# Kernel optimization log

Measured on AMD Instinct MI355X. Metric: run time of the kernel, lower is better.

Reference implementation:

```python
import jax, jax.numpy as jnp
import numpy as np

N = 100_000      # nodes
DEG = 16         # avg in-degree (fixed per node for setup)
E = N * DEG      # edges
IN = 256         # in_feats
H = 4            # num_heads
D = 64           # out_feats per head
NEG_SLOPE = 0.2


def setup_inputs() -> dict:
    key = jax.random.key(0)
    k1, k2, k3, k4, k5 = jax.random.split(key, 5)
    # dst-major CSR with uniform degree DEG per destination node
    row_ptr = jnp.arange(N + 1, dtype=jnp.int32) * DEG          # [N+1]
    col_ind = jax.random.randint(k1, (E,), 0, N, dtype=jnp.int32)  # source ids per edge
    feat = jax.random.normal(k2, (N, IN), dtype=jnp.float32)
    # fc.weight (xavier-ish scale), torch Linear: y = x @ W.T
    W = jax.random.normal(k3, (H * D, IN), dtype=jnp.float32) * (1.0 / np.sqrt(IN))
    attn_l = jax.random.normal(k4, (1, H, D), dtype=jnp.float32) * 0.1
    attn_r = jax.random.normal(k5, (1, H, D), dtype=jnp.float32) * 0.1
    return {"row_ptr": row_ptr, "col_ind": col_ind, "feat": feat,
            "W": W, "attn_l": attn_l, "attn_r": attn_r}


def reference(row_ptr, col_ind, feat, W, attn_l, attn_r):
    n_nodes = feat.shape[0]
    n_edges = col_ind.shape[0]
    # feat_src = feat_dst = fc(feat).view(-1, H, D)
    feat_src = (feat @ W.T).reshape(n_nodes, H, D)
    el = jnp.sum(feat_src * attn_l, axis=-1)   # [N, H]
    er = jnp.sum(feat_src * attn_r, axis=-1)   # [N, H]
    # per-edge dst id from CSR row_ptr; src = col_ind
    dst = (jnp.searchsorted(row_ptr, jnp.arange(n_edges, dtype=row_ptr.dtype),
                            side='right') - 1).astype(jnp.int32)
    src = col_ind
    # e = u_add_v(g, er, el) -> er[src] + el[dst], then LeakyReLU
    e = er[src] + el[dst]                      # [E, H]
    e = jnp.where(e > 0, e, NEG_SLOPE * e)
    # CSR edge-softmax: normalize over incoming edges of each dst row
    m = jax.ops.segment_max(e, dst, num_segments=n_nodes)    # [N, H]
    ex = jnp.exp(e - m[dst])
    s = jax.ops.segment_sum(ex, dst, num_segments=n_nodes)   # [N, H]
    a = ex / s[dst]                                          # [E, H]
    # multi-head SpMM: out[n,h] = sum_{e: dst=n} a[e,h] * feat_src[src[e],h]
    outs = []
    for h in range(H):  # small fixed head loop to avoid [E,H,D] intermediate
        msg = a[:, h, None] * feat_src[src, h]               # [E, D]
        outs.append(jax.ops.segment_sum(msg, dst, num_segments=n_nodes))
    return jnp.stack(outs, axis=1)                           # [N, H, D]
```

## Files before the change

### kernel.cpp

```cpp
#include <hip/hip_runtime.h>
#include <math.h>


#define HEADS 4
#define KIN 256
#define NOUT 256
#define NEG_SLOPE 0.2f
#define BK 32
#define SA 40
#define SB 40

typedef __attribute__((ext_vector_type(4))) short short4v;
typedef __attribute__((ext_vector_type(8))) short short8v;
typedef __attribute__((ext_vector_type(4))) float floatx4;

static __device__ __forceinline__ unsigned short f2bf(float x) {
  unsigned u = __float_as_uint(x);
  u += 0x7FFFu + ((u >> 16) & 1u);
  return (unsigned short)(u >> 16);
}
static __device__ __forceinline__ float bf2f(unsigned short b) {
  return __uint_as_float(((unsigned)b) << 16);
}

__global__ __launch_bounds__(256) void k_cast_w(const float* __restrict__ W,
                                                unsigned short* __restrict__ Wbf) {
  const int i = blockIdx.x * 256 + threadIdx.x;
  float4 f = ((const float4*)W)[i];
  ushort4 o;
  o.x = f2bf(f.x); o.y = f2bf(f.y); o.z = f2bf(f.z); o.w = f2bf(f.w);
  ((ushort4*)Wbf)[i] = o;
}

__global__ __launch_bounds__(256) void k_gemm_mfma(
    const float* __restrict__ feat, const unsigned short* __restrict__ Wbf,
    const float* __restrict__ attn_l, const float* __restrict__ attn_r,
    unsigned short* __restrict__ fs_bf, float* __restrict__ el,
    float* __restrict__ er, int n_nodes) {
  __shared__ unsigned short Alds[64 * SA];
  __shared__ unsigned short Blds[256 * SB];

  const int tid = threadIdx.x;
  const int lane = tid & 63;
  const int w = tid >> 6;
  const int m0 = blockIdx.x * 64;
  const int q = lane >> 4;
  const int l15 = lane & 15;

  floatx4 acc[4][4];
#pragma unroll
  for (int mt = 0; mt < 4; ++mt)
#pragma unroll
    for (int nt = 0; nt < 4; ++nt)
#pragma unroll
      for (int r = 0; r < 4; ++r) acc[mt][nt][r] = 0.0f;

  const int a_row = tid >> 3;
  const int a_kk = (tid & 7) * 4;

  for (int kc = 0; kc < 8; ++kc) {
    const int k0 = kc * BK;
#pragma unroll
    for (int half = 0; half < 2; ++half) {
      const int row = a_row + half * 32;
      int gr = m0 + row;
      if (gr >= n_nodes) gr = n_nodes - 1;
      float4 f = *(const float4*)(feat + (size_t)gr * KIN + k0 + a_kk);
      uint2 p;
      p.x = ((unsigned)f2bf(f.y) << 16) | f2bf(f.x);
      p.y = ((unsigned)f2bf(f.w) << 16) | f2bf(f.z);
      *(uint2*)(&Alds[row * SA + a_kk]) = p;
    }
    {
      const uint4* src = (const uint4*)(Wbf + (size_t)tid * KIN + k0);
      uint2* dst = (uint2*)(&Blds[tid * SB]);
#pragma unroll
      for (int i = 0; i < 4; ++i) {
        uint4 v = src[i];
        dst[2 * i + 0] = make_uint2(v.x, v.y);
        dst[2 * i + 1] = make_uint2(v.z, v.w);
      }
    }
    __syncthreads();
    short8v af[4], bfr[4];
#pragma unroll
    for (int mt = 0; mt < 4; ++mt) {
      const unsigned short* p = &Alds[(mt * 16 + l15) * SA + q * 8];
      short4v lo = *(const short4v*)p;
      short4v hi = *(const short4v*)(p + 4);
      af[mt] = __builtin_shufflevector(lo, hi, 0, 1, 2, 3, 4, 5, 6, 7);
    }
#pragma unroll
    for (int nt = 0; nt < 4; ++nt) {
      const unsigned short* p = &Blds[(w * 64 + nt * 16 + l15) * SB + q * 8];
      short4v lo = *(const short4v*)p;
      short4v hi = *(const short4v*)(p + 4);
      bfr[nt] = __builtin_shufflevector(lo, hi, 0, 1, 2, 3, 4, 5, 6, 7);
    }
#pragma unroll
    for (int mt = 0; mt < 4; ++mt)
#pragma unroll
      for (int nt = 0; nt < 4; ++nt)
        acc[mt][nt] = __builtin_amdgcn_mfma_f32_16x16x32_bf16(
            af[mt], bfr[nt], acc[mt][nt], 0, 0, 0);
    __syncthreads();
  }

  float alv[4], arv[4];
#pragma unroll
  for (int nt = 0; nt < 4; ++nt) {
    alv[nt] = attn_l[w * 64 + nt * 16 + l15];
    arv[nt] = attn_r[w * 64 + nt * 16 + l15];
  }
#pragma unroll
  for (int mt = 0; mt < 4; ++mt) {
#pragma unroll
    for (int r = 0; r < 4; ++r) {
      const int m = m0 + mt * 16 + q * 4 + r;
      const bool mvalid = (m < n_nodes);
      float pl = 0.f, pr = 0.f;
#pragma unroll
      for (int nt = 0; nt < 4; ++nt) {
        const float v = acc[mt][nt][r];
        pl = fmaf(v, alv[nt], pl);
        pr = fmaf(v, arv[nt], pr);
        if (mvalid)
          fs_bf[(size_t)m * NOUT + w * 64 + nt * 16 + l15] = f2bf(v);
      }
#pragma unroll
      for (int off = 1; off < 16; off <<= 1) {
        pl += __shfl_xor(pl, off, 64);
        pr += __shfl_xor(pr, off, 64);
      }
      if (l15 == 0 && mvalid) {
        el[m * HEADS + w] = pl;
        er[m * HEADS + w] = pr;
      }
    }
  }
}

__global__ __launch_bounds__(256) void k_aggregate(
    const int* __restrict__ row_ptr, const int* __restrict__ col_ind,
    const float* __restrict__ el, const float* __restrict__ er,
    const unsigned short* __restrict__ fs_bf, float* __restrict__ out,
    int n_nodes) {
  const int gid = blockIdx.x * blockDim.x + threadIdx.x;
  const int node = gid >> 6;
  const int lane = threadIdx.x & 63;
  if (node >= n_nodes) return;

  const int h = lane >> 4;
  const int j = lane & 15;
  const int rs = row_ptr[node];
  const int deg = row_ptr[node + 1] - rs;

  const bool valid = (j < deg);
  const int src = valid ? col_ind[rs + j] : 0;

  float e = valid ? (er[src * HEADS + h] + el[node * HEADS + h]) : -INFINITY;
  e = (e > 0.f) ? e : NEG_SLOPE * e;

  float mx = e;
#pragma unroll
  for (int off = 1; off < 16; off <<= 1) mx = fmaxf(mx, __shfl_xor(mx, off, 64));
  float ex = valid ? __expf(e - mx) : 0.f;
  float s = ex;
#pragma unroll
  for (int off = 1; off < 16; off <<= 1) s += __shfl_xor(s, off, 64);
  const float a = ex / s;

  const ushort4* __restrict__ fs4 = (const ushort4*)fs_bf;
  const int hbase = lane & 48;
  float4 acc = make_float4(0.f, 0.f, 0.f, 0.f);
#pragma unroll
  for (int j2 = 0; j2 < 16; ++j2) {
    const int sj = __shfl(src, j2, 64);
    const float wgt = __shfl(a, hbase + j2, 64);
    const ushort4 u = fs4[(size_t)sj * (NOUT / 4) + lane];
    acc.x = fmaf(wgt, bf2f(u.x), acc.x);
    acc.y = fmaf(wgt, bf2f(u.y), acc.y);
    acc.z = fmaf(wgt, bf2f(u.z), acc.z);
    acc.w = fmaf(wgt, bf2f(u.w), acc.w);
  }
  ((float4*)out)[(size_t)node * (NOUT / 4) + lane] = acc;
}

extern "C" void kernel_launch(void* const* d_in, const int* in_sizes, int n_in,
                              void* d_out, int out_size, void* d_ws, size_t ws_size,
                              hipStream_t stream) {
  const int* row_ptr = (const int*)d_in[0];
  const int* col_ind = (const int*)d_in[1];
  const float* feat = (const float*)d_in[2];
  const float* W = (const float*)d_in[3];
  const float* attn_l = (const float*)d_in[4];
  const float* attn_r = (const float*)d_in[5];
  float* out = (float*)d_out;
  const int n_nodes = in_sizes[0] - 1;

  char* ws = (char*)d_ws;
  unsigned short* Wbf = (unsigned short*)ws;
  unsigned short* fs_bf = (unsigned short*)(ws + 128 * 1024);
  size_t fs_bytes = (size_t)n_nodes * NOUT * sizeof(unsigned short);
  float* el = (float*)(ws + 128 * 1024 + fs_bytes);
  float* er = el + (size_t)n_nodes * HEADS;

  k_cast_w<<<64, 256, 0, stream>>>(W, Wbf);
  k_gemm_mfma<<<(n_nodes + 63) / 64, 256, 0, stream>>>(
      feat, Wbf, attn_l, attn_r, fs_bf, el, er, n_nodes);
  k_aggregate<<<(n_nodes + 3) / 4, 256, 0, stream>>>(
      row_ptr, col_ind, el, er, fs_bf, out, n_nodes);
}
```

Measured before the change: 360.4 us.

## Restructure GEMM to per-wave 16-row tiles with direct global operand loads

The projection GEMM no longer stages A and B through LDS with block barriers. Each wave now owns 16 rows and computes all 256 output columns, loading feat rows and bf16 W fragments straight from global memory (W should stay cache-resident). Results are staged through a per-wave LDS buffer so fs_bf is written with coalesced 16-byte stores, and el/er are computed for all heads per wave. The aggregate kernel's output store becomes nontemporal, and launch bounds request two blocks per CU. The risk is higher register pressure from 16 accumulators and repeated W loads from L2 for every wave.

```diff
diff --git a/kernel.cpp b/kernel.cpp
--- a/kernel.cpp
+++ b/kernel.cpp
@@ -6,11 +6,8 @@
 #define KIN 256
 #define NOUT 256
 #define NEG_SLOPE 0.2f
-#define BK 32
-#define SA 40
-#define SB 40
+#define SR 280
 
-typedef __attribute__((ext_vector_type(4))) short short4v;
 typedef __attribute__((ext_vector_type(8))) short short8v;
 typedef __attribute__((ext_vector_type(4))) float floatx4;
 
@@ -32,111 +29,95 @@
   ((ushort4*)Wbf)[i] = o;
 }
 
-__global__ __launch_bounds__(256) void k_gemm_mfma(
+__global__ __launch_bounds__(256, 2) void k_gemm_mfma(
     const float* __restrict__ feat, const unsigned short* __restrict__ Wbf,
     const float* __restrict__ attn_l, const float* __restrict__ attn_r,
     unsigned short* __restrict__ fs_bf, float* __restrict__ el,
     float* __restrict__ er, int n_nodes) {
-  __shared__ unsigned short Alds[64 * SA];
-  __shared__ unsigned short Blds[256 * SB];
+  __shared__ unsigned short R[4 * 16 * SR];
 
   const int tid = threadIdx.x;
   const int lane = tid & 63;
   const int w = tid >> 6;
-  const int m0 = blockIdx.x * 64;
   const int q = lane >> 4;
   const int l15 = lane & 15;
+  const int m0 = blockIdx.x * 64 + w * 16;
 
-  floatx4 acc[4][4];
+  int arow_i = m0 + l15;
+  if (arow_i >= n_nodes) arow_i = n_nodes - 1;
+  const float* __restrict__ arow = feat + (size_t)arow_i * KIN;
+
+  floatx4 acc[16];
 #pragma unroll
-  for (int mt = 0; mt < 4; ++mt)
+  for (int nt = 0; nt < 16; ++nt) acc[nt] = (floatx4)0.f;
+
 #pragma unroll
-    for (int nt = 0; nt < 4; ++nt)
+  for (int kc = 0; kc < 8; ++kc) {
+    const int k0 = kc * 32 + q * 8;
+    float4 a0 = *(const float4*)(arow + k0);
+    float4 a1 = *(const float4*)(arow + k0 + 4);
+    short8v af;
+    af[0] = f2bf(a0.x); af[1] = f2bf(a0.y); af[2] = f2bf(a0.z); af[3] = f2bf(a0.w);
+    af[4] = f2bf(a1.x); af[5] = f2bf(a1.y); af[6] = f2bf(a1.z); af[7] = f2bf(a1.w);
 #pragma unroll
-      for (int r = 0; r < 4; ++r) acc[mt][nt][r] = 0.0f;
-
-  const int a_row = tid >> 3;
-  const int a_kk = (tid & 7) * 4;
-
-  for (int kc = 0; kc < 8; ++kc) {
-    const int k0 = kc * BK;
-#pragma unroll
-    for (int half = 0; half < 2; ++half) {
-      const int row = a_row + half * 32;
-      int gr = m0 + row;
-      if (gr >= n_nodes) gr = n_nodes - 1;
-      float4 f = *(const float4*)(feat + (size_t)gr * KIN + k0 + a_kk);
-      uint2 p;
-      p.x = ((unsigned)f2bf(f.y) << 16) | f2bf(f.x);
-      p.y = ((unsigned)f2bf(f.w) << 16) | f2bf(f.z);
-      *(uint2*)(&Alds[row * SA + a_kk]) = p;
+    for (int nt = 0; nt < 16; ++nt) {
+      short8v bf = *(const short8v*)(Wbf + (size_t)(nt * 16 + l15) * KIN + k0);
+      acc[nt] = __builtin_amdgcn_mfma_f32_16x16x32_bf16(af, bf, acc[nt], 0, 0, 0);
     }
-    {
-      const uint4* src = (const uint4*)(Wbf + (size_t)tid * KIN + k0);
-      uint2* dst = (uint2*)(&Blds[tid * SB]);
-#pragma unroll
-      for (int i = 0; i < 4; ++i) {
-        uint4 v = src[i];
-        dst[2 * i + 0] = make_uint2(v.x, v.y);
-        dst[2 * i + 1] = make_uint2(v.z, v.w);
-      }
-    }
-    __syncthreads();
-    short8v af[4], bfr[4];
-#pragma unroll
-    for (int mt = 0; mt < 4; ++mt) {
-      const unsigned short* p = &Alds[(mt * 16 + l15) * SA + q * 8];
-      short4v lo = *(const short4v*)p;
-      short4v hi = *(const short4v*)(p + 4);
-      af[mt] = __builtin_shufflevector(lo, hi, 0, 1, 2, 3, 4, 5, 6, 7);
-    }
-#pragma unroll
-    for (int nt = 0; nt < 4; ++nt) {
-      const unsigned short* p = &Blds[(w * 64 + nt * 16 + l15) * SB + q * 8];
-      short4v lo = *(const short4v*)p;
-      short4v hi = *(const short4v*)(p + 4);
-      bfr[nt] = __builtin_shufflevector(lo, hi, 0, 1, 2, 3, 4, 5, 6, 7);
-    }
-#pragma unroll
-    for (int mt = 0; mt < 4; ++mt)
-#pragma unroll
-      for (int nt = 0; nt < 4; ++nt)
-        acc[mt][nt] = __builtin_amdgcn_mfma_f32_16x16x32_bf16(
-            af[mt], bfr[nt], acc[mt][nt], 0, 0, 0);
-    __syncthreads();
   }
 
-  float alv[4], arv[4];
+  float al_[16], ar_[16];
 #pragma unroll
-  for (int nt = 0; nt < 4; ++nt) {
-    alv[nt] = attn_l[w * 64 + nt * 16 + l15];
-    arv[nt] = attn_r[w * 64 + nt * 16 + l15];
+  for (int nt = 0; nt < 16; ++nt) {
+    al_[nt] = attn_l[nt * 16 + l15];
+    ar_[nt] = attn_r[nt * 16 + l15];
   }
 #pragma unroll
-  for (int mt = 0; mt < 4; ++mt) {
+  for (int r = 0; r < 4; ++r) {
+    const int m = m0 + q * 4 + r;
+    float pl[HEADS], pr[HEADS];
 #pragma unroll
-    for (int r = 0; r < 4; ++r) {
-      const int m = m0 + mt * 16 + q * 4 + r;
-      const bool mvalid = (m < n_nodes);
-      float pl = 0.f, pr = 0.f;
+    for (int h = 0; h < HEADS; ++h) {
+      pl[h] = 0.f; pr[h] = 0.f;
 #pragma unroll
-      for (int nt = 0; nt < 4; ++nt) {
-        const float v = acc[mt][nt][r];
-        pl = fmaf(v, alv[nt], pl);
-        pr = fmaf(v, arv[nt], pr);
-        if (mvalid)
-          fs_bf[(size_t)m * NOUT + w * 64 + nt * 16 + l15] = f2bf(v);
+      for (int t = 0; t < 4; ++t) {
+        const int nt = h * 4 + t;
+        const float v = acc[nt][r];
+        pl[h] = fmaf(v, al_[nt], pl[h]);
+        pr[h] = fmaf(v, ar_[nt], pr[h]);
       }
 #pragma unroll
       for (int off = 1; off < 16; off <<= 1) {
-        pl += __shfl_xor(pl, off, 64);
-        pr += __shfl_xor(pr, off, 64);
-      }
-      if (l15 == 0 && mvalid) {
-        el[m * HEADS + w] = pl;
-        er[m * HEADS + w] = pr;
+        pl[h] += __shfl_xor(pl[h], off, 64);
+        pr[h] += __shfl_xor(pr[h], off, 64);
       }
     }
+    if (m < n_nodes && l15 < HEADS) {
+      float vl = pl[0], vr = pr[0];
+      if (l15 == 1) { vl = pl[1]; vr = pr[1]; }
+      else if (l15 == 2) { vl = pl[2]; vr = pr[2]; }
+      else if (l15 == 3) { vl = pl[3]; vr = pr[3]; }
+      el[m * HEADS + l15] = vl;
+      er[m * HEADS + l15] = vr;
+    }
+  }
+
+  unsigned short* Rw = &R[w * 16 * SR];
+#pragma unroll
+  for (int nt = 0; nt < 16; ++nt)
+#pragma unroll
+    for (int r = 0; r < 4; ++r)
+      Rw[(q * 4 + r) * SR + nt * 16 + l15] = f2bf(acc[nt][r]);
+
+  const int rrow = lane >> 5;
+  const int c8 = (lane & 31) * 8;
+#pragma unroll
+  for (int t = 0; t < 8; ++t) {
+    const int row = t * 2 + rrow;
+    const int m = m0 + row;
+    short8v v = *(const short8v*)(&Rw[row * SR + c8]);
+    if (m < n_nodes)
+      *(short8v*)(fs_bf + (size_t)m * NOUT + c8) = v;
   }
 }
 
@@ -172,7 +153,7 @@
 
   const ushort4* __restrict__ fs4 = (const ushort4*)fs_bf;
   const int hbase = lane & 48;
-  float4 acc = make_float4(0.f, 0.f, 0.f, 0.f);
+  floatx4 acc = (floatx4)0.f;
 #pragma unroll
   for (int j2 = 0; j2 < 16; ++j2) {
     const int sj = __shfl(src, j2, 64);
@@ -183,7 +164,7 @@
     acc.z = fmaf(wgt, bf2f(u.z), acc.z);
     acc.w = fmaf(wgt, bf2f(u.w), acc.w);
   }
-  ((float4*)out)[(size_t)node * (NOUT / 4) + lane] = acc;
+  __builtin_nontemporal_store(acc, (floatx4*)out + (size_t)node * (NOUT / 4) + lane);
 }
 
 extern "C" void kernel_launch(void* const* d_in, const int* in_sizes, int n_in,
```

Result: slower. 409.9 us (+13.7%).
